# Kernel optimization log

Hardware: AMD Instinct MI355X
Metric: run time of the kernel (lower is better)

Reference implementation:

```python
import jax, jax.numpy as jnp
import numpy as np

D_MODEL = 1024
D_HIDDEN = 4096
NUM_BANKS = 16
NUM_SELECTED = 2


def setup_inputs() -> dict:
    key = jax.random.key(0)
    ks = jax.random.split(key, 7)
    s = 0.02
    return {
        "tensor": jax.random.normal(ks[0], (4, 1024, D_MODEL), dtype=jnp.float32),
        "Wr": jax.random.normal(ks[1], (D_MODEL, NUM_BANKS), dtype=jnp.float32) * s,
        "br": jnp.zeros((NUM_BANKS,), dtype=jnp.float32),
        "W1": jax.random.normal(ks[2], (NUM_BANKS, D_MODEL, D_HIDDEN), dtype=jnp.float32) * s,
        "b1": jnp.zeros((NUM_BANKS, D_HIDDEN), dtype=jnp.float32),
        "W2": jax.random.normal(ks[3], (NUM_BANKS, D_HIDDEN, D_MODEL), dtype=jnp.float32) * s,
        "b2": jnp.zeros((NUM_BANKS, D_MODEL), dtype=jnp.float32),
    }


def reference(tensor, Wr, br, W1, b1, W2, b2):
    # Router: softmax over banks, keep top-k probabilities (BankSelector)
    logits = jnp.einsum("bsd,de->bse", tensor, Wr) + br          # [B,S,E]
    probs = jax.nn.softmax(logits, axis=-1)
    topv, topi = jax.lax.top_k(probs, NUM_SELECTED)              # [B,S,K]
    # Dense gate [B,S,E]: selected banks carry their router probability,
    # all other banks are zeroed (equivalent to sparse dispatch/combine).
    gate = jnp.sum(jax.nn.one_hot(topi, NUM_BANKS, dtype=tensor.dtype)
                   * topv[..., None], axis=-2)                    # [B,S,E]
    # Banked expert FFN (BankedLinear x2 with ReLU between)
    h = jax.nn.relu(jnp.einsum("bsd,edh->bseh", tensor, W1) + b1)  # [B,S,E,Dh]
    y = jnp.einsum("bseh,ehm->bsem", h, W2) + b2                   # [B,S,E,Dm]
    # Weighted combine across selected banks
    out = jnp.einsum("bse,bsem->bsm", gate, y)                     # [B,S,Dm]
    return out
```

## Files before the change

### kernel.cpp

```cpp
#include <hip/hip_runtime.h>
#include <stdint.h>

#define D_MODEL   1024
#define D_HIDDEN  4096
#define NBANKS    16
#define NTOK      4096

#define BM 128
#define BN 128
#define BK 64

typedef __attribute__((ext_vector_type(8))) short bf16x8;
typedef __attribute__((ext_vector_type(4))) float f32x4;
typedef __attribute__((ext_vector_type(4))) unsigned int u32x4;

__device__ __forceinline__ unsigned short f2bf(float f) {
  unsigned u = __builtin_bit_cast(unsigned, f);
  u += 0x7FFFu + ((u >> 16) & 1u);
  return (unsigned short)(u >> 16);
}

__device__ __forceinline__ unsigned cvtpk(float lo, float hi) {
  unsigned r;
  asm("v_cvt_pk_bf16_f32 %0, %1, %2" : "=v"(r) : "v"(lo), "v"(hi));
  return r;
}

__device__ __forceinline__ int sidx(int r, int k) {
  return (r << 6) + ((((k >> 3) ^ (r & 7)) << 3) | (k & 7));
}

__global__ __launch_bounds__(256) void zero_out_k(float4* __restrict__ out4,
                                                  int* __restrict__ counts) {
  size_t i = (size_t)blockIdx.x * 256 + threadIdx.x;
  out4[i] = make_float4(0.f, 0.f, 0.f, 0.f);
  if (blockIdx.x == 0 && threadIdx.x < NBANKS) counts[threadIdx.x] = 0;
}

__global__ __launch_bounds__(64) void router_k(const float* __restrict__ x,
                                               const float* __restrict__ Wr,
                                               const float* __restrict__ br,
                                               int* __restrict__ topIdx,
                                               float* __restrict__ topGate) {
  const int t = blockIdx.x;
  const int l = threadIdx.x;
  const float* xr = x + (size_t)t * D_MODEL;

  float acc[NBANKS];
#pragma unroll
  for (int e = 0; e < NBANKS; ++e) acc[e] = 0.f;

  for (int d = l; d < D_MODEL; d += 64) {
    const float xv = xr[d];
    const float* wrow = Wr + (size_t)d * NBANKS;
#pragma unroll
    for (int e = 0; e < NBANKS; ++e) acc[e] += xv * wrow[e];
  }
#pragma unroll
  for (int e = 0; e < NBANKS; ++e) {
#pragma unroll
    for (int m = 1; m < 64; m <<= 1) acc[e] += __shfl_xor(acc[e], m, 64);
  }
#pragma unroll
  for (int e = 0; e < NBANKS; ++e) acc[e] += br[e];

  if (l == 0) {
    float mx = acc[0];
#pragma unroll
    for (int e = 1; e < NBANKS; ++e) mx = fmaxf(mx, acc[e]);
    float p[NBANKS];
    float s = 0.f;
#pragma unroll
    for (int e = 0; e < NBANKS; ++e) { p[e] = expf(acc[e] - mx); s += p[e]; }
    int i0 = 0; float v0 = p[0];
#pragma unroll
    for (int e = 1; e < NBANKS; ++e) if (p[e] > v0) { v0 = p[e]; i0 = e; }
    int i1 = -1; float v1 = -1.f;
#pragma unroll
    for (int e = 0; e < NBANKS; ++e) if (e != i0 && p[e] > v1) { v1 = p[e]; i1 = e; }
    const float inv = 1.f / s;
    topIdx[2 * t]     = i0;
    topIdx[2 * t + 1] = i1;
    topGate[2 * t]     = v0 * inv;
    topGate[2 * t + 1] = v1 * inv;
  }
}

__global__ __launch_bounds__(256) void build_lists_k(const int* __restrict__ topIdx,
                                                     const float* __restrict__ topGate,
                                                     int* __restrict__ counts,
                                                     int* __restrict__ rowlist,
                                                     float* __restrict__ gatelist) {
  const int t = blockIdx.x * 256 + threadIdx.x;
  if (t >= NTOK) return;
#pragma unroll
  for (int k = 0; k < 2; ++k) {
    const int e = topIdx[2 * t + k];
    const int p = atomicAdd(&counts[e], 1);
    rowlist[e * NTOK + p]  = t;
    gatelist[e * NTOK + p] = topGate[2 * t + k];
  }
}

__global__ void scan_k(const int* __restrict__ counts, int* __restrict__ bankOff) {
  if (threadIdx.x == 0) {
    int s = 0;
#pragma unroll
    for (int e = 0; e < NBANKS; ++e) { bankOff[e] = s; s += counts[e]; }
    bankOff[NBANKS] = s;
  }
}

__global__ __launch_bounds__(256, 2) void gemm1_k(const float* __restrict__ X,
                                                  const float* __restrict__ W1,
                                                  const float* __restrict__ b1,
                                                  const int* __restrict__ counts,
                                                  const int* __restrict__ bankOff,
                                                  const int* __restrict__ rowlist,
                                                  unsigned short* __restrict__ H) {
  const int e   = blockIdx.z;
  const int cnt = counts[e];
  const int m0  = blockIdx.y * BM;
  if (m0 >= cnt) return;
  const int n0  = blockIdx.x * BN;

  const int tid  = threadIdx.x;
  const int lane = tid & 63;
  const int w    = tid >> 6;
  const int wm   = (w >> 1) * 64;
  const int wn   = (w & 1) * 64;

  __shared__ unsigned short Xs[BM * BK];
  __shared__ unsigned short Ws[BN * BK];

  const int arow = tid >> 1;
  const int akh  = (tid & 1) * 32;
  const int gi   = min(m0 + arow, cnt - 1);
  const int tok  = rowlist[e * NTOK + gi];
  const float* Asrc = X + (size_t)tok * D_MODEL + akh;
  unsigned short* xw[4];
#pragma unroll
  for (int j = 0; j < 4; ++j) xw[j] = &Xs[sidx(arow, akh + 8 * j)];

  const int nrb = 4 * (tid & 7) + 32 * (tid >> 6);
  const int kb  = 8 * ((tid >> 3) & 7);
  const float* Bsrc = W1 + (size_t)e * D_MODEL * D_HIDDEN + (size_t)kb * D_HIDDEN + n0 + nrb;
  unsigned short* ww[4];
#pragma unroll
  for (int i = 0; i < 4; ++i) ww[i] = &Ws[sidx(nrb + i, kb)];

  const int fr = lane & 15;
  const int fc = (lane >> 4) * 8;

  float raf[8][4];
  float rbf[8][4];

  f32x4 acc[4][4];
#pragma unroll
  for (int i = 0; i < 4; ++i)
#pragma unroll
    for (int j = 0; j < 4; ++j)
#pragma unroll
      for (int r = 0; r < 4; ++r) acc[i][j][r] = 0.f;

  auto LOAD = [&](int t) {
    const float* ap = Asrc + t * BK;
#pragma unroll
    for (int j = 0; j < 8; ++j)
      *(float4*)&raf[j][0] = *(const float4*)(ap + 4 * j);
    const float* bp = Bsrc + (size_t)t * BK * D_HIDDEN;
#pragma unroll
    for (int kk = 0; kk < 8; ++kk)
      *(float4*)&rbf[kk][0] = *(const float4*)(bp + (size_t)kk * D_HIDDEN);
  };

  auto WRITE = [&]() {
#pragma unroll
    for (int j = 0; j < 4; ++j) {
      u32x4 v;
      v[0] = cvtpk(raf[2*j][0], raf[2*j][1]);
      v[1] = cvtpk(raf[2*j][2], raf[2*j][3]);
      v[2] = cvtpk(raf[2*j+1][0], raf[2*j+1][1]);
      v[3] = cvtpk(raf[2*j+1][2], raf[2*j+1][3]);
      *(u32x4*)xw[j] = v;
    }
#pragma unroll
    for (int i = 0; i < 4; ++i) {
      u32x4 v;
      v[0] = cvtpk(rbf[0][i], rbf[1][i]);
      v[1] = cvtpk(rbf[2][i], rbf[3][i]);
      v[2] = cvtpk(rbf[4][i], rbf[5][i]);
      v[3] = cvtpk(rbf[6][i], rbf[7][i]);
      *(u32x4*)ww[i] = v;
    }
  };

  auto COMPUTE = [&]() {
#pragma unroll
    for (int h = 0; h < 2; ++h) {
      bf16x8 af[4], bb[4];
#pragma unroll
      for (int mb = 0; mb < 4; ++mb)
        af[mb] = *(const bf16x8*)&Xs[sidx(wm + mb * 16 + fr, h * 32 + fc)];
#pragma unroll
      for (int nb = 0; nb < 4; ++nb)
        bb[nb] = *(const bf16x8*)&Ws[sidx(wn + nb * 16 + fr, h * 32 + fc)];
#pragma unroll
      for (int mb = 0; mb < 4; ++mb)
#pragma unroll
        for (int nb = 0; nb < 4; ++nb)
          acc[mb][nb] = __builtin_amdgcn_mfma_f32_16x16x32_bf16(af[mb], bb[nb], acc[mb][nb], 0, 0, 0);
    }
  };

  const int NT = D_MODEL / BK;
  LOAD(0);
  WRITE();
  __syncthreads();
#pragma unroll 1
  for (int t = 0; t < NT; ++t) {
    if (t + 1 < NT) LOAD(t + 1);
    COMPUTE();
    __syncthreads();
    if (t + 1 < NT) { WRITE(); __syncthreads(); }
  }

  const int hb = bankOff[e] + m0;
  const int rq = (lane >> 4) * 4;
#pragma unroll
  for (int nb = 0; nb < 4; ++nb) {
    const int col = n0 + wn + nb * 16 + fr;
    const float bias = b1[e * D_HIDDEN + col];
#pragma unroll
    for (int mb = 0; mb < 4; ++mb)
#pragma unroll
      for (int r = 0; r < 4; ++r) {
        const int rowT = wm + mb * 16 + rq + r;
        if (m0 + rowT < cnt) {
          float v = acc[mb][nb][r] + bias;
          v = fmaxf(v, 0.f);
          H[(size_t)(hb + rowT) * D_HIDDEN + col] = f2bf(v);
        }
      }
  }
}

__global__ __launch_bounds__(256, 2) void gemm2_k(const unsigned short* __restrict__ H,
                                                  const float* __restrict__ W2,
                                                  const float* __restrict__ b2,
                                                  const int* __restrict__ counts,
                                                  const int* __restrict__ bankOff,
                                                  const int* __restrict__ rowlist,
                                                  const float* __restrict__ gatelist,
                                                  float* __restrict__ out) {
  const int e   = blockIdx.z;
  const int cnt = counts[e];
  const int m0  = blockIdx.y * BM;
  if (m0 >= cnt) return;
  const int n0  = blockIdx.x * BN;

  const int tid  = threadIdx.x;
  const int lane = tid & 63;
  const int w    = tid >> 6;
  const int wm   = (w >> 1) * 64;
  const int wn   = (w & 1) * 64;

  __shared__ unsigned short Xs[BM * BK];
  __shared__ unsigned short Ws[BN * BK];

  const int arow = tid >> 1;
  const int akh  = (tid & 1) * 32;
  const int hb   = bankOff[e];
  const int gi   = hb + min(m0 + arow, cnt - 1);
  const unsigned short* Asrc = H + (size_t)gi * D_HIDDEN + akh;
  unsigned short* xw[4];
#pragma unroll
  for (int j = 0; j < 4; ++j) xw[j] = &Xs[sidx(arow, akh + 8 * j)];

  const int nrb = 4 * (tid & 7) + 32 * (tid >> 6);
  const int kb  = 8 * ((tid >> 3) & 7);
  const float* Bsrc = W2 + (size_t)e * D_HIDDEN * D_MODEL + (size_t)kb * D_MODEL + n0 + nrb;
  unsigned short* ww[4];
#pragma unroll
  for (int i = 0; i < 4; ++i) ww[i] = &Ws[sidx(nrb + i, kb)];

  const int fr = lane & 15;
  const int fc = (lane >> 4) * 8;

  bf16x8 ha[4];
  float rbf[8][4];

  f32x4 acc[4][4];
#pragma unroll
  for (int i = 0; i < 4; ++i)
#pragma unroll
    for (int j = 0; j < 4; ++j)
#pragma unroll
      for (int r = 0; r < 4; ++r) acc[i][j][r] = 0.f;

  auto LOAD = [&](int t) {
    const unsigned short* ap = Asrc + t * BK;
#pragma unroll
    for (int j = 0; j < 4; ++j) ha[j] = *(const bf16x8*)(ap + 8 * j);
    const float* bp = Bsrc + (size_t)t * BK * D_MODEL;
#pragma unroll
    for (int kk = 0; kk < 8; ++kk)
      *(float4*)&rbf[kk][0] = *(const float4*)(bp + (size_t)kk * D_MODEL);
  };

  auto WRITE = [&]() {
#pragma unroll
    for (int j = 0; j < 4; ++j) *(bf16x8*)xw[j] = ha[j];
#pragma unroll
    for (int i = 0; i < 4; ++i) {
      u32x4 v;
      v[0] = cvtpk(rbf[0][i], rbf[1][i]);
      v[1] = cvtpk(rbf[2][i], rbf[3][i]);
      v[2] = cvtpk(rbf[4][i], rbf[5][i]);
      v[3] = cvtpk(rbf[6][i], rbf[7][i]);
      *(u32x4*)ww[i] = v;
    }
  };

  auto COMPUTE = [&]() {
#pragma unroll
    for (int h = 0; h < 2; ++h) {
      bf16x8 af[4], bb[4];
#pragma unroll
      for (int mb = 0; mb < 4; ++mb)
        af[mb] = *(const bf16x8*)&Xs[sidx(wm + mb * 16 + fr, h * 32 + fc)];
#pragma unroll
      for (int nb = 0; nb < 4; ++nb)
        bb[nb] = *(const bf16x8*)&Ws[sidx(wn + nb * 16 + fr, h * 32 + fc)];
#pragma unroll
      for (int mb = 0; mb < 4; ++mb)
#pragma unroll
        for (int nb = 0; nb < 4; ++nb)
          acc[mb][nb] = __builtin_amdgcn_mfma_f32_16x16x32_bf16(af[mb], bb[nb], acc[mb][nb], 0, 0, 0);
    }
  };

  const int NT = D_HIDDEN / BK;
  LOAD(0);
  WRITE();
  __syncthreads();
#pragma unroll 1
  for (int t = 0; t < NT; ++t) {
    if (t + 1 < NT) LOAD(t + 1);
    COMPUTE();
    __syncthreads();
    if (t + 1 < NT) { WRITE(); __syncthreads(); }
  }

  const int rq = (lane >> 4) * 4;
  float bias[4];
#pragma unroll
  for (int nb = 0; nb < 4; ++nb)
    bias[nb] = b2[e * D_MODEL + n0 + wn + nb * 16 + fr];

#pragma unroll
  for (int mb = 0; mb < 4; ++mb)
#pragma unroll
    for (int r = 0; r < 4; ++r) {
      const int rowT = wm + mb * 16 + rq + r;
      if (m0 + rowT < cnt) {
        const int sidx2 = e * NTOK + m0 + rowT;
        const int tok   = rowlist[sidx2];
        const float g   = gatelist[sidx2];
        float* orow = out + (size_t)tok * D_MODEL;
#pragma unroll
        for (int nb = 0; nb < 4; ++nb) {
          const int col = n0 + wn + nb * 16 + fr;
          atomicAdd(&orow[col], g * (acc[mb][nb][r] + bias[nb]));
        }
      }
    }
}

extern "C" void kernel_launch(void* const* d_in, const int* in_sizes, int n_in,
                              void* d_out, int out_size, void* d_ws, size_t ws_size,
                              hipStream_t stream) {
  const float* X  = (const float*)d_in[0];
  const float* Wr = (const float*)d_in[1];
  const float* br = (const float*)d_in[2];
  const float* W1 = (const float*)d_in[3];
  const float* b1 = (const float*)d_in[4];
  const float* W2 = (const float*)d_in[5];
  const float* b2 = (const float*)d_in[6];
  float* out = (float*)d_out;

  char* w = (char*)d_ws;
  int*   topIdx   = (int*)(w);
  float* topGate  = (float*)(w + (32 << 10));
  int*   counts   = (int*)(w + (64 << 10));
  int*   bankOff  = (int*)(w + (64 << 10) + 256);
  int*   rowlist  = (int*)(w + (66 << 10));
  float* gatelist = (float*)(w + (66 << 10) + NBANKS * NTOK * 4);
  unsigned short* H = (unsigned short*)(w + (1 << 20));

  const size_t needed = (size_t)(1 << 20) + (size_t)(NTOK * 2) * D_HIDDEN * 2;
  if (ws_size < needed) return;

  zero_out_k<<<dim3(4096), dim3(256), 0, stream>>>((float4*)out, counts);
  router_k<<<dim3(NTOK), dim3(64), 0, stream>>>(X, Wr, br, topIdx, topGate);
  build_lists_k<<<dim3(16), dim3(256), 0, stream>>>(topIdx, topGate, counts, rowlist, gatelist);
  scan_k<<<dim3(1), dim3(64), 0, stream>>>(counts, bankOff);
  gemm1_k<<<dim3(D_HIDDEN / BN, NTOK / BM, NBANKS), dim3(256), 0, stream>>>(
      X, W1, b1, counts, bankOff, rowlist, H);
  gemm2_k<<<dim3(D_MODEL / BN, NTOK / BM, NBANKS), dim3(256), 0, stream>>>(
      H, W2, b2, counts, bankOff, rowlist, gatelist, out);
}
```

Baseline: 535.6 us.

## Double-buffer LDS with BK=32 and pre-convert X to bf16

Both expert GEMMs now use a ping-pong shared-memory buffer with a 32-wide K tile. The next tile is written to the alternate buffer during compute, which removes one barrier per iteration. A new kernel converts X to bf16 once up front, so gemm1 loads half the bytes for the A operand and skips per-tile conversion. The swizzle is adjusted for the narrower rows. Trade-offs are twice as many loop iterations with less MFMA work per barrier, and an extra full pass over X.

```diff
diff --git a/kernel.cpp b/kernel.cpp
--- a/kernel.cpp
+++ b/kernel.cpp
@@ -8,11 +8,13 @@
 
 #define BM 128
 #define BN 128
-#define BK 64
+#define BK 32
+#define TBUF (BM * BK)
 
 typedef __attribute__((ext_vector_type(8))) short bf16x8;
 typedef __attribute__((ext_vector_type(4))) float f32x4;
 typedef __attribute__((ext_vector_type(4))) unsigned int u32x4;
+typedef __attribute__((ext_vector_type(2))) unsigned int u32x2;
 
 __device__ __forceinline__ unsigned short f2bf(float f) {
   unsigned u = __builtin_bit_cast(unsigned, f);
@@ -27,7 +29,7 @@
 }
 
 __device__ __forceinline__ int sidx(int r, int k) {
-  return (r << 6) + ((((k >> 3) ^ (r & 7)) << 3) | (k & 7));
+  return (r << 5) + ((((k >> 3) ^ ((r >> 2) & 3)) << 3) | (k & 7));
 }
 
 __global__ __launch_bounds__(256) void zero_out_k(float4* __restrict__ out4,
@@ -35,6 +37,17 @@
   size_t i = (size_t)blockIdx.x * 256 + threadIdx.x;
   out4[i] = make_float4(0.f, 0.f, 0.f, 0.f);
   if (blockIdx.x == 0 && threadIdx.x < NBANKS) counts[threadIdx.x] = 0;
+}
+
+__global__ __launch_bounds__(256) void cvtx_k(const float* __restrict__ X,
+                                              unsigned short* __restrict__ Xb) {
+  const size_t i = ((size_t)blockIdx.x * 256 + threadIdx.x) * 8;
+  const float4 a = *(const float4*)(X + i);
+  const float4 b = *(const float4*)(X + i + 4);
+  u32x4 v;
+  v[0] = cvtpk(a.x, a.y); v[1] = cvtpk(a.z, a.w);
+  v[2] = cvtpk(b.x, b.y); v[3] = cvtpk(b.z, b.w);
+  *(u32x4*)(Xb + i) = v;
 }
 
 __global__ __launch_bounds__(64) void router_k(const float* __restrict__ x,
@@ -111,7 +124,7 @@
   }
 }
 
-__global__ __launch_bounds__(256, 2) void gemm1_k(const float* __restrict__ X,
+__global__ __launch_bounds__(256, 2) void gemm1_k(const unsigned short* __restrict__ Xb,
                                                   const float* __restrict__ W1,
                                                   const float* __restrict__ b1,
                                                   const int* __restrict__ counts,
@@ -130,30 +143,35 @@
   const int wm   = (w >> 1) * 64;
   const int wn   = (w & 1) * 64;
 
-  __shared__ unsigned short Xs[BM * BK];
-  __shared__ unsigned short Ws[BN * BK];
+  __shared__ unsigned short Xs[2 * TBUF];
+  __shared__ unsigned short Ws[2 * TBUF];
 
   const int arow = tid >> 1;
-  const int akh  = (tid & 1) * 32;
+  const int ak   = (tid & 1) * 16;
   const int gi   = min(m0 + arow, cnt - 1);
   const int tok  = rowlist[e * NTOK + gi];
-  const float* Asrc = X + (size_t)tok * D_MODEL + akh;
-  unsigned short* xw[4];
-#pragma unroll
-  for (int j = 0; j < 4; ++j) xw[j] = &Xs[sidx(arow, akh + 8 * j)];
-
-  const int nrb = 4 * (tid & 7) + 32 * (tid >> 6);
-  const int kb  = 8 * ((tid >> 3) & 7);
-  const float* Bsrc = W1 + (size_t)e * D_MODEL * D_HIDDEN + (size_t)kb * D_HIDDEN + n0 + nrb;
-  unsigned short* ww[4];
-#pragma unroll
-  for (int i = 0; i < 4; ++i) ww[i] = &Ws[sidx(nrb + i, kb)];
+  const unsigned short* Asrc = Xb + (size_t)tok * D_MODEL + ak;
+  const int xo0 = sidx(arow, ak);
+  const int xo1 = sidx(arow, ak + 8);
+
+  const int n4 = 4 * (tid & 31);
+  const int k4 = 4 * (tid >> 5);
+  const float* Bsrc = W1 + (size_t)e * D_MODEL * D_HIDDEN + (size_t)k4 * D_HIDDEN + n0 + n4;
+  int wo[4];
+#pragma unroll
+  for (int i = 0; i < 4; ++i) wo[i] = sidx(n4 + i, k4);
 
   const int fr = lane & 15;
   const int fc = (lane >> 4) * 8;
-
-  float raf[8][4];
-  float rbf[8][4];
+  int aoff[4], boff[4];
+#pragma unroll
+  for (int i = 0; i < 4; ++i) {
+    aoff[i] = sidx(wm + i * 16 + fr, fc);
+    boff[i] = sidx(wn + i * 16 + fr, fc);
+  }
+
+  bf16x8 ra0, ra1;
+  float rbf[4][4];
 
   f32x4 acc[4][4];
 #pragma unroll
@@ -163,66 +181,57 @@
 #pragma unroll
       for (int r = 0; r < 4; ++r) acc[i][j][r] = 0.f;
 
+  unsigned short* xc = &Xs[0];       unsigned short* wc = &Ws[0];
+  unsigned short* xn = &Xs[TBUF];    unsigned short* wn_ = &Ws[TBUF];
+
   auto LOAD = [&](int t) {
-    const float* ap = Asrc + t * BK;
-#pragma unroll
-    for (int j = 0; j < 8; ++j)
-      *(float4*)&raf[j][0] = *(const float4*)(ap + 4 * j);
+    const unsigned short* ap = Asrc + t * BK;
+    ra0 = *(const bf16x8*)(ap);
+    ra1 = *(const bf16x8*)(ap + 8);
     const float* bp = Bsrc + (size_t)t * BK * D_HIDDEN;
 #pragma unroll
-    for (int kk = 0; kk < 8; ++kk)
+    for (int kk = 0; kk < 4; ++kk)
       *(float4*)&rbf[kk][0] = *(const float4*)(bp + (size_t)kk * D_HIDDEN);
   };
 
-  auto WRITE = [&]() {
-#pragma unroll
-    for (int j = 0; j < 4; ++j) {
-      u32x4 v;
-      v[0] = cvtpk(raf[2*j][0], raf[2*j][1]);
-      v[1] = cvtpk(raf[2*j][2], raf[2*j][3]);
-      v[2] = cvtpk(raf[2*j+1][0], raf[2*j+1][1]);
-      v[3] = cvtpk(raf[2*j+1][2], raf[2*j+1][3]);
-      *(u32x4*)xw[j] = v;
-    }
+  auto WRITE = [&](unsigned short* xs, unsigned short* ws) {
+    *(bf16x8*)(xs + xo0) = ra0;
+    *(bf16x8*)(xs + xo1) = ra1;
 #pragma unroll
     for (int i = 0; i < 4; ++i) {
-      u32x4 v;
+      u32x2 v;
       v[0] = cvtpk(rbf[0][i], rbf[1][i]);
       v[1] = cvtpk(rbf[2][i], rbf[3][i]);
-      v[2] = cvtpk(rbf[4][i], rbf[5][i]);
-      v[3] = cvtpk(rbf[6][i], rbf[7][i]);
-      *(u32x4*)ww[i] = v;
+      *(u32x2*)(ws + wo[i]) = v;
     }
   };
 
-  auto COMPUTE = [&]() {
-#pragma unroll
-    for (int h = 0; h < 2; ++h) {
-      bf16x8 af[4], bb[4];
-#pragma unroll
-      for (int mb = 0; mb < 4; ++mb)
-        af[mb] = *(const bf16x8*)&Xs[sidx(wm + mb * 16 + fr, h * 32 + fc)];
+  auto COMPUTE = [&](const unsigned short* xs, const unsigned short* ws) {
+    bf16x8 af[4], bb[4];
+#pragma unroll
+    for (int mb = 0; mb < 4; ++mb) af[mb] = *(const bf16x8*)(xs + aoff[mb]);
+#pragma unroll
+    for (int nb = 0; nb < 4; ++nb) bb[nb] = *(const bf16x8*)(ws + boff[nb]);
+#pragma unroll
+    for (int mb = 0; mb < 4; ++mb)
 #pragma unroll
       for (int nb = 0; nb < 4; ++nb)
-        bb[nb] = *(const bf16x8*)&Ws[sidx(wn + nb * 16 + fr, h * 32 + fc)];
-#pragma unroll
-      for (int mb = 0; mb < 4; ++mb)
-#pragma unroll
-        for (int nb = 0; nb < 4; ++nb)
-          acc[mb][nb] = __builtin_amdgcn_mfma_f32_16x16x32_bf16(af[mb], bb[nb], acc[mb][nb], 0, 0, 0);
-    }
+        acc[mb][nb] = __builtin_amdgcn_mfma_f32_16x16x32_bf16(af[mb], bb[nb], acc[mb][nb], 0, 0, 0);
   };
 
   const int NT = D_MODEL / BK;
   LOAD(0);
-  WRITE();
+  WRITE(xc, wc);
   __syncthreads();
 #pragma unroll 1
   for (int t = 0; t < NT; ++t) {
     if (t + 1 < NT) LOAD(t + 1);
-    COMPUTE();
+    __builtin_amdgcn_sched_barrier(0);
+    COMPUTE(xc, wc);
+    if (t + 1 < NT) WRITE(xn, wn_);
     __syncthreads();
-    if (t + 1 < NT) { WRITE(); __syncthreads(); }
+    unsigned short* t0 = xc; xc = xn;  xn  = t0;
+    unsigned short* t1 = wc; wc = wn_; wn_ = t1;
   }
 
   const int hb = bankOff[e] + m0;
@@ -265,30 +274,35 @@
   const int wm   = (w >> 1) * 64;
   const int wn   = (w & 1) * 64;
 
-  __shared__ unsigned short Xs[BM * BK];
-  __shared__ unsigned short Ws[BN * BK];
+  __shared__ unsigned short Xs[2 * TBUF];
+  __shared__ unsigned short Ws[2 * TBUF];
 
   const int arow = tid >> 1;
-  const int akh  = (tid & 1) * 32;
+  const int ak   = (tid & 1) * 16;
   const int hb   = bankOff[e];
   const int gi   = hb + min(m0 + arow, cnt - 1);
-  const unsigned short* Asrc = H + (size_t)gi * D_HIDDEN + akh;
-  unsigned short* xw[4];
-#pragma unroll
-  for (int j = 0; j < 4; ++j) xw[j] = &Xs[sidx(arow, akh + 8 * j)];
-
-  const int nrb = 4 * (tid & 7) + 32 * (tid >> 6);
-  const int kb  = 8 * ((tid >> 3) & 7);
-  const float* Bsrc = W2 + (size_t)e * D_HIDDEN * D_MODEL + (size_t)kb * D_MODEL + n0 + nrb;
-  unsigned short* ww[4];
-#pragma unroll
-  for (int i = 0; i < 4; ++i) ww[i] = &Ws[sidx(nrb + i, kb)];
+  const unsigned short* Asrc = H + (size_t)gi * D_HIDDEN + ak;
+  const int xo0 = sidx(arow, ak);
+  const int xo1 = sidx(arow, ak + 8);
+
+  const int n4 = 4 * (tid & 31);
+  const int k4 = 4 * (tid >> 5);
+  const float* Bsrc = W2 + (size_t)e * D_HIDDEN * D_MODEL + (size_t)k4 * D_MODEL + n0 + n4;
+  int wo[4];
+#pragma unroll
+  for (int i = 0; i < 4; ++i) wo[i] = sidx(n4 + i, k4);
 
   const int fr = lane & 15;
   const int fc = (lane >> 4) * 8;
-
-  bf16x8 ha[4];
-  float rbf[8][4];
+  int aoff[4], boff[4];
+#pragma unroll
+  for (int i = 0; i < 4; ++i) {
+    aoff[i] = sidx(wm + i * 16 + fr, fc);
+    boff[i] = sidx(wn + i * 16 + fr, fc);
+  }
+
+  bf16x8 ra0, ra1;
+  float rbf[4][4];
 
   f32x4 acc[4][4];
 #pragma unroll
@@ -297,59 +311,58 @@
     for (int j = 0; j < 4; ++j)
 #pragma unroll
       for (int r = 0; r < 4; ++r) acc[i][j][r] = 0.f;
+
+  unsigned short* xc = &Xs[0];       unsigned short* wc = &Ws[0];
+  unsigned short* xn = &Xs[TBUF];    unsigned short* wn_ = &Ws[TBUF];
 
   auto LOAD = [&](int t) {
     const unsigned short* ap = Asrc + t * BK;
-#pragma unroll
-    for (int j = 0; j < 4; ++j) ha[j] = *(const bf16x8*)(ap + 8 * j);
+    ra0 = *(const bf16x8*)(ap);
+    ra1 = *(const bf16x8*)(ap + 8);
     const float* bp = Bsrc + (size_t)t * BK * D_MODEL;
 #pragma unroll
-    for (int kk = 0; kk < 8; ++kk)
+    for (int kk = 0; kk < 4; ++kk)
       *(float4*)&rbf[kk][0] = *(const float4*)(bp + (size_t)kk * D_MODEL);
   };
 
-  auto WRITE = [&]() {
-#pragma unroll
-    for (int j = 0; j < 4; ++j) *(bf16x8*)xw[j] = ha[j];
+  auto WRITE = [&](unsigned short* xs, unsigned short* ws) {
+    *(bf16x8*)(xs + xo0) = ra0;
+    *(bf16x8*)(xs + xo1) = ra1;
 #pragma unroll
     for (int i = 0; i < 4; ++i) {
-      u32x4 v;
+      u32x2 v;
       v[0] = cvtpk(rbf[0][i], rbf[1][i]);
       v[1] = cvtpk(rbf[2][i], rbf[3][i]);
-      v[2] = cvtpk(rbf[4][i], rbf[5][i]);
-      v[3] = cvtpk(rbf[6][i], rbf[7][i]);
-      *(u32x4*)ww[i] = v;
+      *(u32x2*)(ws + wo[i]) = v;
     }
   };
 
-  auto COMPUTE = [&]() {
-#pragma unroll
-    for (int h = 0; h < 2; ++h) {
-      bf16x8 af[4], bb[4];
-#pragma unroll
-      for (int mb = 0; mb < 4; ++mb)
-        af[mb] = *(const bf16x8*)&Xs[sidx(wm + mb * 16 + fr, h * 32 + fc)];
+  auto COMPUTE = [&](const unsigned short* xs, const unsigned short* ws) {
+    bf16x8 af[4], bb[4];
+#pragma unroll
+    for (int mb = 0; mb < 4; ++mb) af[mb] = *(const bf16x8*)(xs + aoff[mb]);
+#pragma unroll
+    for (int nb = 0; nb < 4; ++nb) bb[nb] = *(const bf16x8*)(ws + boff[nb]);
+#pragma unroll
+    for (int mb = 0; mb < 4; ++mb)
 #pragma unroll
       for (int nb = 0; nb < 4; ++nb)
-        bb[nb] = *(const bf16x8*)&Ws[sidx(wn + nb * 16 + fr, h * 32 + fc)];
-#pragma unroll
-      for (int mb = 0; mb < 4; ++mb)
-#pragma unroll
-        for (int nb = 0; nb < 4; ++nb)
-          acc[mb][nb] = __builtin_amdgcn_mfma_f32_16x16x32_bf16(af[mb], bb[nb], acc[mb][nb], 0, 0, 0);
-    }
+        acc[mb][nb] = __builtin_amdgcn_mfma_f32_16x16x32_bf16(af[mb], bb[nb], acc[mb][nb], 0, 0, 0);
   };
 
   const int NT = D_HIDDEN / BK;
   LOAD(0);
-  WRITE();
+  WRITE(xc, wc);
   __syncthreads();
 #pragma unroll 1
   for (int t = 0; t < NT; ++t) {
     if (t + 1 < NT) LOAD(t + 1);
-    COMPUTE();
+    __builtin_amdgcn_sched_barrier(0);
+    COMPUTE(xc, wc);
+    if (t + 1 < NT) WRITE(xn, wn_);
     __syncthreads();
-    if (t + 1 < NT) { WRITE(); __syncthreads(); }
+    unsigned short* t0 = xc; xc = xn;  xn  = t0;
+    unsigned short* t1 = wc; wc = wn_; wn_ = t1;
   }
 
   const int rq = (lane >> 4) * 4;
@@ -364,9 +377,9 @@
     for (int r = 0; r < 4; ++r) {
       const int rowT = wm + mb * 16 + rq + r;
       if (m0 + rowT < cnt) {
-        const int sidx2 = e * NTOK + m0 + rowT;
-        const int tok   = rowlist[sidx2];
-        const float g   = gatelist[sidx2];
+        const int si = e * NTOK + m0 + rowT;
+        const int tok = rowlist[si];
+        const float g = gatelist[si];
         float* orow = out + (size_t)tok * D_MODEL;
 #pragma unroll
         for (int nb = 0; nb < 4; ++nb) {
@@ -396,17 +409,19 @@
   int*   bankOff  = (int*)(w + (64 << 10) + 256);
   int*   rowlist  = (int*)(w + (66 << 10));
   float* gatelist = (float*)(w + (66 << 10) + NBANKS * NTOK * 4);
-  unsigned short* H = (unsigned short*)(w + (1 << 20));
-
-  const size_t needed = (size_t)(1 << 20) + (size_t)(NTOK * 2) * D_HIDDEN * 2;
+  unsigned short* Xb = (unsigned short*)(w + (1 << 20));
+  unsigned short* H  = (unsigned short*)(w + (16 << 20));
+
+  const size_t needed = (size_t)(16 << 20) + (size_t)(NTOK * 2) * D_HIDDEN * 2;
   if (ws_size < needed) return;
 
   zero_out_k<<<dim3(4096), dim3(256), 0, stream>>>((float4*)out, counts);
+  cvtx_k<<<dim3(NTOK * D_MODEL / 8 / 256), dim3(256), 0, stream>>>(X, Xb);
   router_k<<<dim3(NTOK), dim3(64), 0, stream>>>(X, Wr, br, topIdx, topGate);
   build_lists_k<<<dim3(16), dim3(256), 0, stream>>>(topIdx, topGate, counts, rowlist, gatelist);
   scan_k<<<dim3(1), dim3(64), 0, stream>>>(counts, bankOff);
   gemm1_k<<<dim3(D_HIDDEN / BN, NTOK / BM, NBANKS), dim3(256), 0, stream>>>(
-      X, W1, b1, counts, bankOff, rowlist, H);
+      Xb, W1, b1, counts, bankOff, rowlist, H);
   gemm2_k<<<dim3(D_MODEL / BN, NTOK / BM, NBANKS), dim3(256), 0, stream>>>(
       H, W2, b2, counts, bankOff, rowlist, gatelist, out);
 }
```

Result: faster. 478.6 us (-10.6%).
